# Kernel tuning notes

Hardware: AMD Instinct MI355X
Metric: run time of the kernel (lower is better)

The kernel has to match this reference:

```python
import jax, jax.numpy as jnp
import numpy as np

# Graph sizes
B, N, E = 8, 512, 262144          # graphs, nodes/graph, total edges
ND, ED, GD = 128, 64, 32          # node, edge, glob feature dims
FIN = 2 * ND + ED                 # 320 = msg('sr') + existing edges
CTX = GD                          # ctxt_dim = 0, ctxt is globs only
H1, OUT = 256, 64                 # feat_net hidden / output (== ED for 'add' residual)
AH, NHEADS = 64, 4                # attn_net hidden / heads
HEAD = OUT // NHEADS              # 16
EPS = 1e-5


def setup_inputs() -> dict:
    key = jax.random.key(0)
    ks = jax.random.split(key, 12)
    nodes = jax.random.normal(ks[0], (B, N, ND), jnp.float32)
    edges0 = jax.random.normal(ks[1], (E, ED), jnp.float32)
    globs = jax.random.normal(ks[2], (B, GD), jnp.float32)
    batch_idx = jnp.sort(jax.random.randint(ks[3], (E,), 0, B, jnp.int32))
    send_idx = jax.random.randint(ks[4], (E,), 0, N, jnp.int32)
    recv_idx = jax.random.randint(ks[5], (E,), 0, N, jnp.int32)
    # LayerNorm params over feat_inpt_dim
    ln_g = jnp.ones((FIN,), jnp.float32)
    ln_b = jnp.zeros((FIN,), jnp.float32)
    # feat_net: 2-layer SiLU MLP, ctxt concatenated at the input
    W1 = 0.05 * jax.random.normal(ks[6], (FIN + CTX, H1), jnp.float32)
    b1 = jnp.zeros((H1,), jnp.float32)
    W2 = 0.05 * jax.random.normal(ks[7], (H1, OUT), jnp.float32)
    b2 = jnp.zeros((OUT,), jnp.float32)
    # attn_net: 2-layer SiLU MLP -> n_heads scores
    A1 = 0.05 * jax.random.normal(ks[8], (FIN + CTX, AH), jnp.float32)
    ab1 = jnp.zeros((AH,), jnp.float32)
    A2 = 0.05 * jax.random.normal(ks[9], (AH, NHEADS), jnp.float32)
    ab2 = jnp.zeros((NHEADS,), jnp.float32)
    return dict(nodes=nodes, edges0=edges0, globs=globs, ln_g=ln_g, ln_b=ln_b,
                W1=W1, b1=b1, W2=W2, b2=b2, A1=A1, ab1=ab1, A2=A2, ab2=ab2,
                batch_idx=batch_idx, send_idx=send_idx, recv_idx=recv_idx)


def reference(nodes, edges0, globs, ln_g, ln_b, W1, b1, W2, b2, A1, ab1, A2, ab2,
              batch_idx, send_idx, recv_idx):
    # Build messages: gather sender/receiver node feats per edge ('sr')
    send = nodes[batch_idx, send_idx]                      # [E, ND]
    recv = nodes[batch_idx, recv_idx]                      # [E, ND]
    feats = jnp.concatenate([edges0, send, recv], axis=-1)  # [E, FIN]
    # Pre-LN
    mu = feats.mean(-1, keepdims=True)
    var = feats.var(-1, keepdims=True)
    feats = (feats - mu) * jax.lax.rsqrt(var + EPS) * ln_g + ln_b
    # Broadcast per-graph globals to edges (ctxt_from_mask)
    x = jnp.concatenate([feats, globs[batch_idx]], axis=-1)  # [E, FIN+CTX]
    # Attention scores / sqrt(feat_outp_dim)
    a = (jax.nn.silu(x @ A1 + ab1) @ A2 + ab2) / np.sqrt(OUT)  # [E, NHEADS]
    # Segment softmax over the sender dim (group by (graph, receiver))
    seg = batch_idx * N + recv_idx
    nseg = B * N
    amax = jax.ops.segment_max(a, seg, num_segments=nseg)
    amax = jnp.where(jnp.isfinite(amax), amax, 0.0)
    ae = jnp.exp(a - amax[seg])
    denom = jax.ops.segment_sum(ae, seg, num_segments=nseg)
    attn = ae / denom[seg]                                  # [E, NHEADS]
    attn = jnp.repeat(attn, HEAD, axis=-1)                  # [E, OUT]
    # Edge feature update + additive residual
    new_edges = jax.nn.silu(x @ W1 + b1) @ W2 + b2 + edges0  # [E, OUT]
    # Attention-weighted scatter-sum pool over senders, zeros for isolated nodes
    pooled = jax.ops.segment_sum(new_edges * attn, seg, num_segments=nseg)
    pooled = pooled.reshape(B, N, OUT)
    return new_edges, pooled
```

## Files before the change

kernel.cpp:

```cpp
#include <hip/hip_runtime.h>
#include <hip/hip_bf16.h>
#include <cstdint>

typedef __bf16 bf16;
typedef __bf16 bf16x8 __attribute__((ext_vector_type(8)));
typedef float f32x4 __attribute__((ext_vector_type(4)));

#define E_TOT   262144
#define NNODE   512
#define NDIM    128
#define EDIM    64
#define GDIM    32
#define FIN     320
#define XD      352
#define H1D     256
#define OUTD    64
#define AHD     64
#define NHEADS  4
#define NSEG    4096
#define TE      48

#define SX_STR  360
#define SH_STR  264
#define SA_STR  72

#define PRM_LNG 0
#define PRM_LNB 320
#define PRM_B1  640
#define PRM_B2  896
#define PRM_A2  960
#define PRM_AB1 1216
#define PRM_AB2 1280
#define PRM_TOT 1284

#define SMEM_SX    0
#define SMEM_SA    25600
#define SMEM_SCORE 34560
#define SMEM_A2    35328
#define SMEM_LNG   36352
#define SMEM_LNB   37632
#define SMEM_IDX   38912
#define SMEM_TOT   39680

__device__ __forceinline__ float siluf(float v) {
    return v / (1.0f + __expf(-v));
}

__device__ __forceinline__ bool probe_bf16(const void* nodes, int t) {
    const unsigned short* u16 = (const unsigned short*)nodes;
    int lane = t & 63;
    int pl = 0;
    #pragma unroll
    for (int i = 0; i < 4; i++) {
        unsigned short u = u16[lane * 4 + i];
        int expo = (u >> 7) & 0xFF;
        pl += (((u & 0x7FFF) == 0) || (expo >= 97 && expo <= 137)) ? 1 : 0;
    }
    #pragma unroll
    for (int m = 1; m < 64; m <<= 1) pl += __shfl_xor(pl, m);
    return pl >= 240;
}

__global__ __launch_bounds__(256) void k_prep(
    const void* __restrict__ nodes,
    const void* __restrict__ W1, const void* __restrict__ W2, const void* __restrict__ A1,
    const void* __restrict__ ln_g, const void* __restrict__ ln_b,
    const void* __restrict__ b1, const void* __restrict__ b2,
    const void* __restrict__ A2, const void* __restrict__ ab1, const void* __restrict__ ab2,
    bf16* __restrict__ W1T, bf16* __restrict__ W2T, bf16* __restrict__ A1T,
    float* __restrict__ prm) {
    int b = blockIdx.x, t = threadIdx.x;
    bool isb = probe_bf16(nodes, t);
    if (b < 352) {
        int i = b * 256 + t;
        int k = i / H1D, n = i % H1D;
        float v = isb ? (float)((const bf16*)W1)[i] : ((const float*)W1)[i];
        W1T[n * XD + k] = (bf16)v;
    } else if (b < 416) {
        int i = (b - 352) * 256 + t;
        int k = i / OUTD, n = i % OUTD;
        float v = isb ? (float)((const bf16*)W2)[i] : ((const float*)W2)[i];
        W2T[n * H1D + k] = (bf16)v;
    } else if (b < 504) {
        int i = (b - 416) * 256 + t;
        int k = i / AHD, n = i % AHD;
        float v = isb ? (float)((const bf16*)A1)[i] : ((const float*)A1)[i];
        A1T[n * XD + k] = (bf16)v;
    } else {
        int i = (b - 504) * 256 + t;
        if (i < PRM_TOT) {
            const void* src; int off;
            if (i < 320)       { src = ln_g; off = i; }
            else if (i < 640)  { src = ln_b; off = i - 320; }
            else if (i < 896)  { src = b1;   off = i - 640; }
            else if (i < 960)  { src = b2;   off = i - 896; }
            else if (i < 1216) { src = A2;   off = i - 960; }
            else if (i < 1280) { src = ab1;  off = i - 1216; }
            else               { src = ab2;  off = i - 1280; }
            prm[i] = isb ? (float)((const bf16*)src)[off] : ((const float*)src)[off];
        }
    }
}

__global__ __launch_bounds__(256, 4) void k_edge(
    const void* __restrict__ nodes, const void* __restrict__ edges0,
    const void* __restrict__ globs, const float* __restrict__ prm,
    const int* __restrict__ bidx, const int* __restrict__ sidx,
    const int* __restrict__ ridx,
    const bf16* __restrict__ W1T, const bf16* __restrict__ W2T,
    const bf16* __restrict__ A1T,
    void* __restrict__ outNE, float* __restrict__ denom,
    float* __restrict__ pooled) {

    __shared__ __align__(16) char smem[SMEM_TOT];
    bf16*  sX    = (bf16*)(smem + SMEM_SX);
    bf16*  sH    = (bf16*)(smem + SMEM_SX);
    bf16*  sA    = (bf16*)(smem + SMEM_SA);
    float* sScore= (float*)(smem + SMEM_SCORE);
    float* sA2   = (float*)(smem + SMEM_A2);
    float* sLnG  = (float*)(smem + SMEM_LNG);
    float* sLnB  = (float*)(smem + SMEM_LNB);
    int*   sBi   = (int*)(smem + SMEM_IDX);
    int*   sSi   = sBi + TE;
    int*   sRi   = sBi + 2 * TE;
    int*   sSeg  = sBi + 3 * TE;

    const int t  = threadIdx.x;
    const int e0 = blockIdx.x * TE;
    const int ne = min(TE, E_TOT - e0);
    const bool isb = probe_bf16(nodes, t);

    if (t < TE) {
        int ge = e0 + t;
        if (t < ne) {
            int bi = bidx[ge], si = sidx[ge], ri = ridx[ge];
            sBi[t] = bi; sSi[t] = si; sRi[t] = ri;
            sSeg[t] = bi * NNODE + ri;
        } else {
            sBi[t] = 0; sSi[t] = 0; sRi[t] = 0; sSeg[t] = 0;
        }
    } else if (t < 128) {
        int c = t - 48;
        if (c < 80) ((float4*)sLnG)[c] = ((const float4*)(prm + PRM_LNG))[c];
    } else if (t < 208) {
        int c = t - 128;
        ((float4*)sLnB)[c] = ((const float4*)(prm + PRM_LNB))[c];
    } else {
        int c = t - 208;
        if (c < 32) {
            ((float4*)sA2)[c]      = ((const float4*)(prm + PRM_A2))[c];
            ((float4*)sA2)[c + 32] = ((const float4*)(prm + PRM_A2))[c + 32];
        }
    }
    __syncthreads();

    {
        const int eh = t >> 3, gl = t & 7;
        for (int half = 0; half < 2; half++) {
            const int e = half * 32 + eh;
            if (e >= TE) break;
            if (e >= ne) {
                bf16x8 zz = {};
                #pragma unroll
                for (int j = 0; j < 6; j++) {
                    int c = gl + j * 8;
                    if (c < 44) *(bf16x8*)&sX[e * SX_STR + c * 8] = zz;
                }
                continue;
            }
            const int ge = e0 + e;
            const int bi = sBi[e], si = sSi[e], ri = sRi[e];
            float v[40];
            #pragma unroll
            for (int j = 0; j < 5; j++) {
                const int c = gl + j * 8;
                const void* base; size_t off;
                if (c < 8)       { base = edges0; off = (size_t)ge * EDIM + c * 8; }
                else if (c < 24) { base = nodes;  off = (size_t)(bi * NNODE + si) * NDIM + (c - 8) * 8; }
                else             { base = nodes;  off = (size_t)(bi * NNODE + ri) * NDIM + (c - 24) * 8; }
                if (isb) {
                    bf16x8 x = *(const bf16x8*)((const bf16*)base + off);
                    #pragma unroll
                    for (int ii = 0; ii < 8; ii++) v[j * 8 + ii] = (float)x[ii];
                } else {
                    const float* sf = (const float*)base + off;
                    float4 f0 = ((const float4*)sf)[0];
                    float4 f1 = ((const float4*)sf)[1];
                    v[j*8+0]=f0.x; v[j*8+1]=f0.y; v[j*8+2]=f0.z; v[j*8+3]=f0.w;
                    v[j*8+4]=f1.x; v[j*8+5]=f1.y; v[j*8+6]=f1.z; v[j*8+7]=f1.w;
                }
            }
            float s = 0.f, sq = 0.f;
            #pragma unroll
            for (int ii = 0; ii < 40; ii++) { s += v[ii]; sq += v[ii] * v[ii]; }
            #pragma unroll
            for (int m = 1; m < 8; m <<= 1) { s += __shfl_xor(s, m); sq += __shfl_xor(sq, m); }
            float mean = s * (1.0f / FIN);
            float var  = sq * (1.0f / FIN) - mean * mean;
            float rstd = rsqrtf(var + 1e-5f);
            #pragma unroll
            for (int j = 0; j < 5; j++) {
                const int c = gl + j * 8;
                const float* gP = &sLnG[c * 8];
                const float* bP = &sLnB[c * 8];
                bf16x8 o;
                #pragma unroll
                for (int ii = 0; ii < 8; ii++)
                    o[ii] = (bf16)((v[j * 8 + ii] - mean) * rstd * gP[ii] + bP[ii]);
                *(bf16x8*)&sX[e * SX_STR + c * 8] = o;
            }
            if (gl < 4) {
                const int c = 40 + gl;
                size_t off = (size_t)bi * GDIM + gl * 8;
                bf16x8 o;
                if (isb) {
                    o = *(const bf16x8*)((const bf16*)globs + off);
                } else {
                    const float* sf = (const float*)globs + off;
                    float4 f0 = ((const float4*)sf)[0];
                    float4 f1 = ((const float4*)sf)[1];
                    o[0]=(bf16)f0.x; o[1]=(bf16)f0.y; o[2]=(bf16)f0.z; o[3]=(bf16)f0.w;
                    o[4]=(bf16)f1.x; o[5]=(bf16)f1.y; o[6]=(bf16)f1.z; o[7]=(bf16)f1.w;
                }
                *(bf16x8*)&sX[e * SX_STR + c * 8] = o;
            }
        }
    }
    __syncthreads();

    const int w = t >> 6, lane = t & 63, quad = lane >> 4, l15 = lane & 15;
    f32x4 z = {0.f, 0.f, 0.f, 0.f};

    f32x4 acc[3][4], accA[3];
    #pragma unroll
    for (int s2 = 0; s2 < 3; s2++) { accA[s2] = z; for (int i = 0; i < 4; i++) acc[s2][i] = z; }
    {
        const bf16* pW = W1T + (size_t)(w * 64 + l15) * XD + quad * 8;
        const bf16* pA = A1T + (size_t)(w * 16 + l15) * XD + quad * 8;
        bf16x8 bw[4], ba;
        #pragma unroll
        for (int i = 0; i < 4; i++) bw[i] = *(const bf16x8*)(pW + (size_t)i * 16 * XD);
        ba = *(const bf16x8*)pA;
        for (int kk = 0; kk < 11; kk++) {
            bf16x8 bwn[4], ban;
            if (kk < 10) {
                #pragma unroll
                for (int i = 0; i < 4; i++) bwn[i] = *(const bf16x8*)(pW + (size_t)i * 16 * XD + (kk + 1) * 32);
                ban = *(const bf16x8*)(pA + (kk + 1) * 32);
            }
            const int kc = kk * 32 + quad * 8;
            bf16x8 a[3];
            #pragma unroll
            for (int s2 = 0; s2 < 3; s2++) a[s2] = *(bf16x8*)&sX[(s2 * 16 + l15) * SX_STR + kc];
            #pragma unroll
            for (int i = 0; i < 4; i++)
                #pragma unroll
                for (int s2 = 0; s2 < 3; s2++)
                    acc[s2][i] = __builtin_amdgcn_mfma_f32_16x16x32_bf16(a[s2], bw[i], acc[s2][i], 0, 0, 0);
            #pragma unroll
            for (int s2 = 0; s2 < 3; s2++)
                accA[s2] = __builtin_amdgcn_mfma_f32_16x16x32_bf16(a[s2], ba, accA[s2], 0, 0, 0);
            if (kk < 10) {
                #pragma unroll
                for (int i = 0; i < 4; i++) bw[i] = bwn[i];
                ba = ban;
            }
        }
    }
    __syncthreads();

    #pragma unroll
    for (int i = 0; i < 4; i++) {
        const int n = w * 64 + i * 16 + l15;
        const float bb = prm[PRM_B1 + n];
        #pragma unroll
        for (int s2 = 0; s2 < 3; s2++)
            #pragma unroll
            for (int r = 0; r < 4; r++)
                sH[(s2 * 16 + quad * 4 + r) * SH_STR + n] = (bf16)siluf(acc[s2][i][r] + bb);
    }
    {
        const int n = w * 16 + l15;
        const float ba1 = prm[PRM_AB1 + n];
        #pragma unroll
        for (int s2 = 0; s2 < 3; s2++)
            #pragma unroll
            for (int r = 0; r < 4; r++)
                sA[(s2 * 16 + quad * 4 + r) * SA_STR + n] = (bf16)siluf(accA[s2][r] + ba1);
    }
    __syncthreads();

    if (t < TE * NHEADS) {
        const int e = t >> 2, h = t & 3;
        if (e < ne) {
            float dot = 0.f;
            #pragma unroll
            for (int c = 0; c < 8; c++) {
                bf16x8 v = *(bf16x8*)&sA[e * SA_STR + c * 8];
                #pragma unroll
                for (int ii = 0; ii < 8; ii++)
                    dot += (float)v[ii] * sA2[(c * 8 + ii) * NHEADS + h];
            }
            float ex = __expf((dot + prm[PRM_AB2 + h]) * 0.125f);
            sScore[e * 4 + h] = ex;
            atomicAdd(&denom[sSeg[e] * NHEADS + h], ex);
        }
    }
    __syncthreads();

    {
        f32x4 c2[3] = {z, z, z};
        const int n = w * 16 + l15;
        const bf16* pW2 = W2T + (size_t)n * H1D + quad * 8;
        bf16x8 b2f = *(const bf16x8*)pW2;
        for (int kk = 0; kk < 8; kk++) {
            bf16x8 b2n;
            if (kk < 7) b2n = *(const bf16x8*)(pW2 + (kk + 1) * 32);
            const int kc = kk * 32 + quad * 8;
            #pragma unroll
            for (int s2 = 0; s2 < 3; s2++) {
                bf16x8 a = *(bf16x8*)&sH[(s2 * 16 + l15) * SH_STR + kc];
                c2[s2] = __builtin_amdgcn_mfma_f32_16x16x32_bf16(a, b2f, c2[s2], 0, 0, 0);
            }
            if (kk < 7) b2f = b2n;
        }
        const float bb2 = prm[PRM_B2 + n];
        #pragma unroll
        for (int s2 = 0; s2 < 3; s2++)
            #pragma unroll
            for (int r = 0; r < 4; r++) {
                const int row = s2 * 16 + quad * 4 + r;
                if (row < ne) {
                    size_t off = (size_t)(e0 + row) * EDIM + n;
                    float ev = isb ? (float)((const bf16*)edges0)[off] : ((const float*)edges0)[off];
                    float v = c2[s2][r] + bb2 + ev;
                    if (isb) ((bf16*)outNE)[off] = (bf16)v;
                    else     ((float*)outNE)[off] = v;
                    float ex = sScore[row * 4 + w];
                    atomicAdd(&pooled[(size_t)sSeg[row] * OUTD + n], v * ex);
                }
            }
    }
}

__global__ __launch_bounds__(256) void k_norm(const float* __restrict__ pooled,
                                              const float* __restrict__ denom,
                                              const void* __restrict__ nodes,
                                              void* __restrict__ d_out) {
    int i = blockIdx.x * 256 + threadIdx.x;
    bool isb = probe_bf16(nodes, threadIdx.x);
    int s = i >> 6, j = i & 63, h = j >> 4;
    float den = denom[s * 4 + h];
    float v = (den > 0.f) ? pooled[i] / den : 0.0f;
    size_t po = (size_t)E_TOT * OUTD + i;
    if (isb) ((bf16*)d_out)[po] = (bf16)v;
    else     ((float*)d_out)[po] = v;
}

static char* align_up(char* p, size_t a) {
    return (char*)(((uintptr_t)p + (a - 1)) & ~(uintptr_t)(a - 1));
}

extern "C" void kernel_launch(void* const* d_in, const int* in_sizes, int n_in,
                              void* d_out, int out_size, void* d_ws, size_t ws_size,
                              hipStream_t stream) {
    const void* nodes  = d_in[0];
    const void* edges0 = d_in[1];
    const void* globs  = d_in[2];
    const void* ln_g   = d_in[3];
    const void* ln_b   = d_in[4];
    const void* W1     = d_in[5];
    const void* b1     = d_in[6];
    const void* W2     = d_in[7];
    const void* b2     = d_in[8];
    const void* A1     = d_in[9];
    const void* ab1    = d_in[10];
    const void* A2     = d_in[11];
    const void* ab2    = d_in[12];
    const int*  bidx   = (const int*)d_in[13];
    const int*  sidx   = (const int*)d_in[14];
    const int*  ridx   = (const int*)d_in[15];

    char* p = (char*)d_ws;
    float*    prm    = (float*)p;    p = align_up(p + PRM_TOT * 4, 256);
    bf16*     W1T    = (bf16*)p;     p = align_up(p + XD * H1D * 2, 256);
    bf16*     W2T    = (bf16*)p;     p = align_up(p + H1D * OUTD * 2, 256);
    bf16*     A1T    = (bf16*)p;     p = align_up(p + XD * AHD * 2, 256);
    float*    denom  = (float*)p;    p += NSEG * NHEADS * 4;
    float*    pooled = (float*)p;    p += (size_t)NSEG * OUTD * 4;

    hipMemsetAsync(denom, 0, NSEG * NHEADS * 4 + (size_t)NSEG * OUTD * 4, stream);
    k_prep<<<dim3(510), dim3(256), 0, stream>>>(
        nodes, W1, W2, A1, ln_g, ln_b, b1, b2, A2, ab1, ab2,
        W1T, W2T, A1T, prm);
    k_edge<<<dim3((E_TOT + TE - 1) / TE), dim3(256), 0, stream>>>(
        nodes, edges0, globs, prm,
        bidx, sidx, ridx, W1T, W2T, A1T, d_out, denom, pooled);
    k_norm<<<dim3(NSEG * OUTD / 256), dim3(256), 0, stream>>>(pooled, denom, nodes, d_out);
}
```

Measured before the change: 345.6 us.

## Fold LayerNorm affine into weights, fuse zeroing into prep, restructure score/pool epilogue

Folds ln_g into the transposed W1/A1 columns and ln_b into precomputed b1/ab1 biases, so the edge kernel skips the per-element affine and its shared-memory tables. Replaces hipMemsetAsync with extra zeroing blocks in k_prep, and drops one __syncthreads by computing attention scores per wave and broadcasting them with shuffles. It also hoists the first W1/A1/W2 fragment loads and edges0 residual loads earlier, adds s_setprio around MFMA bursts, and uses rcp in SiLU. Folding changes the rounding order relative to the reference, and k_prep now does serial 320-length dot products in two blocks.

```diff
diff --git a/kernel.cpp b/kernel.cpp
--- a/kernel.cpp
+++ b/kernel.cpp
@@ -24,26 +24,28 @@
 #define SH_STR  264
 #define SA_STR  72
 
-#define PRM_LNG 0
-#define PRM_LNB 320
-#define PRM_B1  640
-#define PRM_B2  896
-#define PRM_A2  960
-#define PRM_AB1 1216
-#define PRM_AB2 1280
-#define PRM_TOT 1284
+#define PRM_B1  0
+#define PRM_B2  256
+#define PRM_A2  320
+#define PRM_AB1 576
+#define PRM_AB2 640
+#define PRM_TOT 644
 
 #define SMEM_SX    0
 #define SMEM_SA    25600
-#define SMEM_SCORE 34560
-#define SMEM_A2    35328
-#define SMEM_LNG   36352
-#define SMEM_LNB   37632
-#define SMEM_IDX   38912
-#define SMEM_TOT   39680
+#define SMEM_A2T   34560
+#define SMEM_SEG   35584
+#define SMEM_TOT   35776
+
+#define ZOFF 507
+#define ZBLK 272
 
 __device__ __forceinline__ float siluf(float v) {
-    return v / (1.0f + __expf(-v));
+    return v * __builtin_amdgcn_rcpf(1.0f + __expf(-v));
+}
+
+__device__ __forceinline__ float ldf(const void* p, int i, bool isb) {
+    return isb ? (float)((const bf16*)p)[i] : ((const float*)p)[i];
 }
 
 __device__ __forceinline__ bool probe_bf16(const void* nodes, int t) {
@@ -68,37 +70,44 @@
     const void* __restrict__ b1, const void* __restrict__ b2,
     const void* __restrict__ A2, const void* __restrict__ ab1, const void* __restrict__ ab2,
     bf16* __restrict__ W1T, bf16* __restrict__ W2T, bf16* __restrict__ A1T,
-    float* __restrict__ prm) {
+    float* __restrict__ prm, float* __restrict__ denom) {
     int b = blockIdx.x, t = threadIdx.x;
+    if (b >= ZOFF) {
+        float4 z4 = {0.f, 0.f, 0.f, 0.f};
+        ((float4*)denom)[(b - ZOFF) * 256 + t] = z4;
+        return;
+    }
     bool isb = probe_bf16(nodes, t);
     if (b < 352) {
-        int i = b * 256 + t;
-        int k = i / H1D, n = i % H1D;
-        float v = isb ? (float)((const bf16*)W1)[i] : ((const float*)W1)[i];
-        W1T[n * XD + k] = (bf16)v;
+        int o = b * 256 + t;
+        int n = o / XD, k = o - n * XD;
+        float g = (k < FIN) ? ldf(ln_g, k, isb) : 1.0f;
+        W1T[o] = (bf16)(ldf(W1, k * H1D + n, isb) * g);
     } else if (b < 416) {
-        int i = (b - 352) * 256 + t;
-        int k = i / OUTD, n = i % OUTD;
-        float v = isb ? (float)((const bf16*)W2)[i] : ((const float*)W2)[i];
-        W2T[n * H1D + k] = (bf16)v;
+        int o = (b - 352) * 256 + t;
+        int n = o >> 8, k = o & 255;
+        W2T[o] = (bf16)ldf(W2, k * OUTD + n, isb);
     } else if (b < 504) {
-        int i = (b - 416) * 256 + t;
-        int k = i / AHD, n = i % AHD;
-        float v = isb ? (float)((const bf16*)A1)[i] : ((const float*)A1)[i];
-        A1T[n * XD + k] = (bf16)v;
+        int o = (b - 416) * 256 + t;
+        int n = o / XD, k = o - n * XD;
+        float g = (k < FIN) ? ldf(ln_g, k, isb) : 1.0f;
+        A1T[o] = (bf16)(ldf(A1, k * AHD + n, isb) * g);
+    } else if (b == 504) {
+        float acc = ldf(b1, t, isb);
+        #pragma unroll 4
+        for (int k = 0; k < FIN; k++) acc += ldf(ln_b, k, isb) * ldf(W1, k * H1D + t, isb);
+        prm[PRM_B1 + t] = acc;
+    } else if (b == 505) {
+        if (t < AHD) {
+            float acc = ldf(ab1, t, isb);
+            #pragma unroll 4
+            for (int k = 0; k < FIN; k++) acc += ldf(ln_b, k, isb) * ldf(A1, k * AHD + t, isb);
+            prm[PRM_AB1 + t] = acc;
+        }
     } else {
-        int i = (b - 504) * 256 + t;
-        if (i < PRM_TOT) {
-            const void* src; int off;
-            if (i < 320)       { src = ln_g; off = i; }
-            else if (i < 640)  { src = ln_b; off = i - 320; }
-            else if (i < 896)  { src = b1;   off = i - 640; }
-            else if (i < 960)  { src = b2;   off = i - 896; }
-            else if (i < 1216) { src = A2;   off = i - 960; }
-            else if (i < 1280) { src = ab1;  off = i - 1216; }
-            else               { src = ab2;  off = i - 1280; }
-            prm[i] = isb ? (float)((const bf16*)src)[off] : ((const float*)src)[off];
-        }
+        if (t < 64)        prm[PRM_B2 + t] = ldf(b2, t, isb);
+        else if (t < 320)  prm[PRM_A2 + t - 64] = ldf(A2, t - 64, isb);
+        else if (t < 324)  prm[PRM_AB2 + t - 320] = ldf(ab2, t - 320, isb);
     }
 }
 
@@ -116,43 +125,24 @@
     bf16*  sX    = (bf16*)(smem + SMEM_SX);
     bf16*  sH    = (bf16*)(smem + SMEM_SX);
     bf16*  sA    = (bf16*)(smem + SMEM_SA);
-    float* sScore= (float*)(smem + SMEM_SCORE);
-    float* sA2   = (float*)(smem + SMEM_A2);
-    float* sLnG  = (float*)(smem + SMEM_LNG);
-    float* sLnB  = (float*)(smem + SMEM_LNB);
-    int*   sBi   = (int*)(smem + SMEM_IDX);
-    int*   sSi   = sBi + TE;
-    int*   sRi   = sBi + 2 * TE;
-    int*   sSeg  = sBi + 3 * TE;
+    float* sA2T  = (float*)(smem + SMEM_A2T);
+    int*   sSeg  = (int*)(smem + SMEM_SEG);
 
     const int t  = threadIdx.x;
     const int e0 = blockIdx.x * TE;
     const int ne = min(TE, E_TOT - e0);
     const bool isb = probe_bf16(nodes, t);
 
-    if (t < TE) {
-        int ge = e0 + t;
-        if (t < ne) {
-            int bi = bidx[ge], si = sidx[ge], ri = ridx[ge];
-            sBi[t] = bi; sSi[t] = si; sRi[t] = ri;
-            sSeg[t] = bi * NNODE + ri;
-        } else {
-            sBi[t] = 0; sSi[t] = 0; sRi[t] = 0; sSeg[t] = 0;
-        }
-    } else if (t < 128) {
-        int c = t - 48;
-        if (c < 80) ((float4*)sLnG)[c] = ((const float4*)(prm + PRM_LNG))[c];
-    } else if (t < 208) {
-        int c = t - 128;
-        ((float4*)sLnB)[c] = ((const float4*)(prm + PRM_LNB))[c];
-    } else {
-        int c = t - 208;
-        if (c < 32) {
-            ((float4*)sA2)[c]      = ((const float4*)(prm + PRM_A2))[c];
-            ((float4*)sA2)[c + 32] = ((const float4*)(prm + PRM_A2))[c + 32];
-        }
-    }
-    __syncthreads();
+    const int w = t >> 6, lane = t & 63, quad = lane >> 4, l15 = lane & 15;
+
+    const bf16* pW = W1T + (size_t)(w * 64 + l15) * XD + quad * 8;
+    const bf16* pA = A1T + (size_t)(w * 16 + l15) * XD + quad * 8;
+    bf16x8 bw[4], ba;
+    #pragma unroll
+    for (int i = 0; i < 4; i++) bw[i] = *(const bf16x8*)(pW + (size_t)i * 16 * XD);
+    ba = *(const bf16x8*)pA;
+
+    { int h = t >> 6, k = t & 63; sA2T[h * 64 + k] = prm[PRM_A2 + k * 4 + h] * 0.125f; }
 
     {
         const int eh = t >> 3, gl = t & 7;
@@ -169,7 +159,8 @@
                 continue;
             }
             const int ge = e0 + e;
-            const int bi = sBi[e], si = sSi[e], ri = sRi[e];
+            const int bi = bidx[ge], si = sidx[ge], ri = ridx[ge];
+            if (gl == 0) sSeg[e] = bi * NNODE + ri;
             float v[40];
             #pragma unroll
             for (int j = 0; j < 5; j++) {
@@ -201,12 +192,10 @@
             #pragma unroll
             for (int j = 0; j < 5; j++) {
                 const int c = gl + j * 8;
-                const float* gP = &sLnG[c * 8];
-                const float* bP = &sLnB[c * 8];
                 bf16x8 o;
                 #pragma unroll
                 for (int ii = 0; ii < 8; ii++)
-                    o[ii] = (bf16)((v[j * 8 + ii] - mean) * rstd * gP[ii] + bP[ii]);
+                    o[ii] = (bf16)((v[j * 8 + ii] - mean) * rstd);
                 *(bf16x8*)&sX[e * SX_STR + c * 8] = o;
             }
             if (gl < 4) {
@@ -228,19 +217,12 @@
     }
     __syncthreads();
 
-    const int w = t >> 6, lane = t & 63, quad = lane >> 4, l15 = lane & 15;
     f32x4 z = {0.f, 0.f, 0.f, 0.f};
 
     f32x4 acc[3][4], accA[3];
     #pragma unroll
     for (int s2 = 0; s2 < 3; s2++) { accA[s2] = z; for (int i = 0; i < 4; i++) acc[s2][i] = z; }
     {
-        const bf16* pW = W1T + (size_t)(w * 64 + l15) * XD + quad * 8;
-        const bf16* pA = A1T + (size_t)(w * 16 + l15) * XD + quad * 8;
-        bf16x8 bw[4], ba;
-        #pragma unroll
-        for (int i = 0; i < 4; i++) bw[i] = *(const bf16x8*)(pW + (size_t)i * 16 * XD);
-        ba = *(const bf16x8*)pA;
         for (int kk = 0; kk < 11; kk++) {
             bf16x8 bwn[4], ban;
             if (kk < 10) {
@@ -252,6 +234,7 @@
             bf16x8 a[3];
             #pragma unroll
             for (int s2 = 0; s2 < 3; s2++) a[s2] = *(bf16x8*)&sX[(s2 * 16 + l15) * SX_STR + kc];
+            __builtin_amdgcn_s_setprio(1);
             #pragma unroll
             for (int i = 0; i < 4; i++)
                 #pragma unroll
@@ -260,6 +243,7 @@
             #pragma unroll
             for (int s2 = 0; s2 < 3; s2++)
                 accA[s2] = __builtin_amdgcn_mfma_f32_16x16x32_bf16(a[s2], ba, accA[s2], 0, 0, 0);
+            __builtin_amdgcn_s_setprio(0);
             if (kk < 10) {
                 #pragma unroll
                 for (int i = 0; i < 4; i++) bw[i] = bwn[i];
@@ -288,59 +272,69 @@
             for (int r = 0; r < 4; r++)
                 sA[(s2 * 16 + quad * 4 + r) * SA_STR + n] = (bf16)siluf(accA[s2][r] + ba1);
     }
+    const int n2 = w * 16 + l15;
+    const bf16* pW2 = W2T + (size_t)n2 * H1D + quad * 8;
+    bf16x8 b2f = *(const bf16x8*)pW2;
     __syncthreads();
 
-    if (t < TE * NHEADS) {
-        const int e = t >> 2, h = t & 3;
-        if (e < ne) {
-            float dot = 0.f;
-            #pragma unroll
-            for (int c = 0; c < 8; c++) {
-                bf16x8 v = *(bf16x8*)&sA[e * SA_STR + c * 8];
-                #pragma unroll
-                for (int ii = 0; ii < 8; ii++)
-                    dot += (float)v[ii] * sA2[(c * 8 + ii) * NHEADS + h];
-            }
-            float ex = __expf((dot + prm[PRM_AB2 + h]) * 0.125f);
-            sScore[e * 4 + h] = ex;
-            atomicAdd(&denom[sSeg[e] * NHEADS + h], ex);
-        }
-    }
-    __syncthreads();
-
+    float score;
     {
-        f32x4 c2[3] = {z, z, z};
-        const int n = w * 16 + l15;
-        const bf16* pW2 = W2T + (size_t)n * H1D + quad * 8;
-        bf16x8 b2f = *(const bf16x8*)pW2;
-        for (int kk = 0; kk < 8; kk++) {
-            bf16x8 b2n;
-            if (kk < 7) b2n = *(const bf16x8*)(pW2 + (kk + 1) * 32);
-            const int kc = kk * 32 + quad * 8;
-            #pragma unroll
-            for (int s2 = 0; s2 < 3; s2++) {
-                bf16x8 a = *(bf16x8*)&sH[(s2 * 16 + l15) * SH_STR + kc];
-                c2[s2] = __builtin_amdgcn_mfma_f32_16x16x32_bf16(a, b2f, c2[s2], 0, 0, 0);
-            }
-            if (kk < 7) b2f = b2n;
-        }
-        const float bb2 = prm[PRM_B2 + n];
-        #pragma unroll
-        for (int s2 = 0; s2 < 3; s2++)
-            #pragma unroll
-            for (int r = 0; r < 4; r++) {
-                const int row = s2 * 16 + quad * 4 + r;
-                if (row < ne) {
-                    size_t off = (size_t)(e0 + row) * EDIM + n;
-                    float ev = isb ? (float)((const bf16*)edges0)[off] : ((const float*)edges0)[off];
-                    float v = c2[s2][r] + bb2 + ev;
-                    if (isb) ((bf16*)outNE)[off] = (bf16)v;
-                    else     ((float*)outNE)[off] = v;
-                    float ex = sScore[row * 4 + w];
-                    atomicAdd(&pooled[(size_t)sSeg[row] * OUTD + n], v * ex);
-                }
-            }
-    }
+        const int eSc = (lane < TE) ? lane : 0;
+        float dot = 0.f;
+        #pragma unroll
+        for (int c = 0; c < 8; c++) {
+            bf16x8 vv = *(bf16x8*)&sA[eSc * SA_STR + c * 8];
+            float4 wa = ((float4*)&sA2T[w * 64 + c * 8])[0];
+            float4 wb = ((float4*)&sA2T[w * 64 + c * 8])[1];
+            dot += (float)vv[0]*wa.x + (float)vv[1]*wa.y + (float)vv[2]*wa.z + (float)vv[3]*wa.w
+                 + (float)vv[4]*wb.x + (float)vv[5]*wb.y + (float)vv[6]*wb.z + (float)vv[7]*wb.w;
+        }
+        score = __expf(dot + prm[PRM_AB2 + w] * 0.125f);
+        if (lane < ne) atomicAdd(&denom[sSeg[lane] * NHEADS + w], score);
+    }
+
+    float ev[3][4], sc[3][4];
+    #pragma unroll
+    for (int s2 = 0; s2 < 3; s2++)
+        #pragma unroll
+        for (int r = 0; r < 4; r++) {
+            const int row = s2 * 16 + quad * 4 + r;
+            sc[s2][r] = __shfl(score, row);
+            if (row < ne) {
+                size_t off = (size_t)(e0 + row) * EDIM + n2;
+                ev[s2][r] = isb ? (float)((const bf16*)edges0)[off] : ((const float*)edges0)[off];
+            } else ev[s2][r] = 0.f;
+        }
+
+    f32x4 c2[3] = {z, z, z};
+    for (int kk = 0; kk < 8; kk++) {
+        bf16x8 b2n;
+        if (kk < 7) b2n = *(const bf16x8*)(pW2 + (kk + 1) * 32);
+        const int kc = kk * 32 + quad * 8;
+        bf16x8 a0 = *(bf16x8*)&sH[l15 * SH_STR + kc];
+        bf16x8 a1 = *(bf16x8*)&sH[(16 + l15) * SH_STR + kc];
+        bf16x8 a2 = *(bf16x8*)&sH[(32 + l15) * SH_STR + kc];
+        __builtin_amdgcn_s_setprio(1);
+        c2[0] = __builtin_amdgcn_mfma_f32_16x16x32_bf16(a0, b2f, c2[0], 0, 0, 0);
+        c2[1] = __builtin_amdgcn_mfma_f32_16x16x32_bf16(a1, b2f, c2[1], 0, 0, 0);
+        c2[2] = __builtin_amdgcn_mfma_f32_16x16x32_bf16(a2, b2f, c2[2], 0, 0, 0);
+        __builtin_amdgcn_s_setprio(0);
+        if (kk < 7) b2f = b2n;
+    }
+    const float bb2 = prm[PRM_B2 + n2];
+    #pragma unroll
+    for (int s2 = 0; s2 < 3; s2++)
+        #pragma unroll
+        for (int r = 0; r < 4; r++) {
+            const int row = s2 * 16 + quad * 4 + r;
+            if (row < ne) {
+                size_t off = (size_t)(e0 + row) * EDIM + n2;
+                float v = c2[s2][r] + bb2 + ev[s2][r];
+                if (isb) ((bf16*)outNE)[off] = (bf16)v;
+                else     ((float*)outNE)[off] = v;
+                atomicAdd(&pooled[(size_t)sSeg[row] * OUTD + n2], v * sc[s2][r]);
+            }
+        }
 }
 
 __global__ __launch_bounds__(256) void k_norm(const float* __restrict__ pooled,
@@ -389,10 +383,9 @@
     float*    denom  = (float*)p;    p += NSEG * NHEADS * 4;
     float*    pooled = (float*)p;    p += (size_t)NSEG * OUTD * 4;
 
-    hipMemsetAsync(denom, 0, NSEG * NHEADS * 4 + (size_t)NSEG * OUTD * 4, stream);
-    k_prep<<<dim3(510), dim3(256), 0, stream>>>(
+    k_prep<<<dim3(ZOFF + ZBLK), dim3(256), 0, stream>>>(
         nodes, W1, W2, A1, ln_g, ln_b, b1, b2, A2, ab1, ab2,
-        W1T, W2T, A1T, prm);
+        W1T, W2T, A1T, prm, denom);
     k_edge<<<dim3((E_TOT + TE - 1) / TE), dim3(256), 0, stream>>>(
         nodes, edges0, globs, prm,
         bidx, sidx, ridx, W1T, W2T, A1T, d_out, denom, pooled);
```

New measurement: 421.1 us. +21.8%, slower.
